# Optimization experiments

Hardware: AMD Instinct MI355X
Metric: run time of the kernel (lower is better)

Reference implementation:

```python
import jax, jax.numpy as jnp
import numpy as np

QB = 127.0  # act_bits=8 -> 2**(8-1)-1
EPS = 1e-5


def _ste(x, q):
    # straight-through estimator: forward = q, backward = identity
    return x + jax.lax.stop_gradient(q - x)


def bitlinear(x, W, b):
    """BitNet-b1.58 linear: ternary weights (per-tensor mean-abs scale),
    8-bit per-token absmax activations, dequantized matmul + bias."""
    w_scale = jnp.clip(jnp.mean(jnp.abs(W)), EPS, None)
    Wq = _ste(W, jnp.clip(jnp.round(W / w_scale), -1.0, 1.0) * w_scale)  # ternary * scale
    x_scale = jnp.clip(jnp.max(jnp.abs(x), axis=-1, keepdims=True), EPS, None)
    xq = _ste(x, jnp.clip(jnp.round(x * (QB / x_scale)), -QB - 1.0, QB) * (x_scale / QB))
    # x: [B, N, d_in], W: [d_out, d_in] -> [B, N, d_out]
    return jnp.einsum('bnd,hd->bnh', xq, Wq) + b


def setup_inputs() -> dict:
    key = jax.random.key(0)
    k0, k1, k2 = jax.random.split(key, 3)
    B, N, D = 8, 4096, 1024
    H = int(D * 4.0)
    x = jax.random.normal(k0, (B, N, D), dtype=jnp.float32)
    W1 = jax.random.normal(k1, (H, D), dtype=jnp.float32) * 0.02
    b1 = jnp.zeros((H,), dtype=jnp.float32)
    W2 = jax.random.normal(k2, (D, H), dtype=jnp.float32) * 0.02
    b2 = jnp.zeros((D,), dtype=jnp.float32)
    return {"x": x, "W1": W1, "b1": b1, "W2": W2, "b2": b2}


def reference(x, W1, b1, W2, b2):
    h = bitlinear(x, W1, b1)                 # [B, N, H]
    h = jax.nn.gelu(h, approximate=False)    # torch nn.GELU default = exact erf
    # dropout with p=0.0 is identity
    return bitlinear(h, W2, b2)              # [B, N, D]
```

## Files before the change

kernel.cpp:

```cpp
#include <hip/hip_runtime.h>
#include <hip/hip_bf16.h>
#include <math.h>


typedef int int32x4 __attribute__((ext_vector_type(4)));

typedef const void __attribute__((address_space(1))) gv_t;
typedef void __attribute__((address_space(3))) lv_t;

__device__ __forceinline__ void gload_lds16(const signed char* g,
                                            signed char* l) {
  __builtin_amdgcn_global_load_lds((gv_t*)g, (lv_t*)l, 16, 0, 0);
}

__device__ __forceinline__ float gelu_erf(float v) {
  return 0.5f * v * (1.0f + erff(v * 0.70710678118654752440f));
}

__device__ __forceinline__ void store_gt(float* p, float v) { *p = v; }
__device__ __forceinline__ void store_gt(__hip_bfloat16* p, float v) {
  unsigned u = __float_as_uint(v);
  u += 0x7fffu + ((u >> 16) & 1u);
  *(unsigned short*)p = (unsigned short)(u >> 16);
}

__device__ __forceinline__ void load4v(const float* p, float v[4]) {
  const float4 t = *(const float4*)p;
  v[0] = t.x; v[1] = t.y; v[2] = t.z; v[3] = t.w;
}
__device__ __forceinline__ void load4v(const __hip_bfloat16* p, float v[4]) {
  const ushort4 t = *(const ushort4*)p;
  v[0] = __uint_as_float((unsigned)t.x << 16);
  v[1] = __uint_as_float((unsigned)t.y << 16);
  v[2] = __uint_as_float((unsigned)t.z << 16);
  v[3] = __uint_as_float((unsigned)t.w << 16);
}

__global__ __launch_bounds__(256) void absmean_partial(
    const float* __restrict__ W, double* __restrict__ part) {
  const int tid = threadIdx.x;
  const long base = (long)blockIdx.x * 8192;
  double s = 0.0;
#pragma unroll
  for (int c = 0; c < 8; ++c) {
    const float4 v = *(const float4*)&W[base + c * 1024 + tid * 4];
    s += (double)fabsf(v.x) + (double)fabsf(v.y) +
         (double)fabsf(v.z) + (double)fabsf(v.w);
  }
  __shared__ double sm[256];
  sm[tid] = s; __syncthreads();
  for (int off = 128; off; off >>= 1) {
    if (tid < off) sm[tid] += sm[tid + off];
    __syncthreads();
  }
  if (tid == 0) part[blockIdx.x] = sm[0];
}

__global__ __launch_bounds__(256) void absmean_final(
    const double* __restrict__ part, double* __restrict__ out, double n) {
  const int tid = threadIdx.x;
  __shared__ double sm[256];
  sm[tid] = part[tid] + part[tid + 256];
  __syncthreads();
  for (int off = 128; off; off >>= 1) {
    if (tid < off) sm[tid] += sm[tid + off];
    __syncthreads();
  }
  if (tid == 0) out[0] = fmax(sm[0] / n, 1e-5);
}

__global__ __launch_bounds__(256) void quant_w(
    const float* __restrict__ W, const double* __restrict__ wsP,
    signed char* __restrict__ Wq) {
  const double ws = *wsP;
  const long i = ((long)blockIdx.x * 256 + threadIdx.x) * 4;
  const float4 v = *(const float4*)&W[i];
  const float vv[4] = {v.x, v.y, v.z, v.w};
  int pack = 0;
#pragma unroll
  for (int q = 0; q < 4; ++q) {
    double r = rint((double)vv[q] / ws);
    r = fmin(fmax(r, -1.0), 1.0);
    pack |= (((int)r) & 0xff) << (8 * q);
  }
  *(int*)&Wq[i] = pack;
}

template <int L, bool GELU, typename GT>
__global__ __launch_bounds__(256) void quant_rows(
    const GT* __restrict__ X, signed char* __restrict__ Xq,
    float* __restrict__ dsc) {
  constexpr int CH = L / 1024;
  const long row = blockIdx.x;
  const int tid = threadIdx.x;
  const GT* xr = X + row * (long)L;
  float v[CH][4];
  float m = 0.f;
#pragma unroll
  for (int c = 0; c < CH; ++c) {
    load4v(xr + c * 1024 + tid * 4, v[c]);
#pragma unroll
    for (int q = 0; q < 4; ++q) {
      if (GELU) v[c][q] = gelu_erf(v[c][q]);
      m = fmaxf(m, fabsf(v[c][q]));
    }
  }
#pragma unroll
  for (int off = 32; off; off >>= 1) m = fmaxf(m, __shfl_down(m, off, 64));
  __shared__ float wmx[4];
  if ((tid & 63) == 0) wmx[tid >> 6] = m;
  __syncthreads();
  float ms = fmaxf(fmaxf(wmx[0], wmx[1]), fmaxf(wmx[2], wmx[3]));
  ms = fmaxf(ms, 1e-5f);
  const double inv = 127.0 / (double)ms;
#pragma unroll
  for (int c = 0; c < CH; ++c) {
    int pack = 0;
#pragma unroll
    for (int q = 0; q < 4; ++q) {
      double r = rint((double)v[c][q] * inv);
      r = fmin(fmax(r, -128.0), 127.0);
      pack |= (((int)r) & 0xff) << (8 * q);
    }
    *(int*)&Xq[row * (long)L + c * 1024 + tid * 4] = pack;
  }
  if (tid == 0) dsc[row] = (float)((double)ms / 127.0);
}

template <typename GT>
__global__ __launch_bounds__(512, 2) void gemm_i8_256(
    const signed char* __restrict__ A, const signed char* __restrict__ Bm,
    const float* __restrict__ dA, const double* __restrict__ wsB,
    const float* __restrict__ bias, GT* __restrict__ C,
    int K, int Ncol, int nx) {
  __shared__ signed char LDS[131072];
  const int tid = threadIdx.x;
  const int lane = tid & 63;
  const int wave = tid >> 6;
  const int wm = wave >> 2;
  const int wn = wave & 3;

  const int cpx = gridDim.x >> 3;
  const int wg = ((int)blockIdx.x & 7) * cpx + ((int)blockIdx.x >> 3);
  const long rowBase = (long)(wg / nx) * 256;
  const long colBase = (long)(wg % nx) * 256;
  const int NT = K >> 6;

  const int d0 = tid << 4;
  const int r0 = d0 >> 6;
  const int c0 = (d0 & 63) ^ (((d0 >> 7) & 3) << 4);
  const signed char* gA0 = A + (rowBase + r0) * (long)K + c0;
  const signed char* gA1 = A + (rowBase + r0 + 128) * (long)K + c0;
  const signed char* gB0 = Bm + (colBase + r0) * (long)K + c0;
  const signed char* gB1 = Bm + (colBase + r0 + 128) * (long)K + c0;

  auto STAGE = [&](int tt) {
    const int bb = (tt & 3) << 14;
    const int k0 = tt << 6;
    gload_lds16(gA0 + k0, &LDS[bb + d0]);
    gload_lds16(gA1 + k0, &LDS[bb + d0 + 8192]);
    gload_lds16(gB0 + k0, &LDS[65536 + bb + d0]);
    gload_lds16(gB1 + k0, &LDS[65536 + bb + d0 + 8192]);
  };

  const int rl = lane & 15;
  const int kc = (lane >> 4) << 4;
  int aoff[8], boff[4];
#pragma unroll
  for (int mi = 0; mi < 8; ++mi) {
    const int a = (wm * 128 + mi * 16 + rl) * 64 + kc;
    aoff[mi] = a ^ (((a >> 7) & 3) << 4);
  }
#pragma unroll
  for (int nj = 0; nj < 4; ++nj) {
    const int a = (wn * 64 + nj * 16 + rl) * 64 + kc;
    boff[nj] = a ^ (((a >> 7) & 3) << 4);
  }

  int32x4 acc[8][4] = {};
  STAGE(0); STAGE(1); STAGE(2);

  for (int t = 0; t < NT; ++t) {
    if (t < NT - 2)       asm volatile("s_waitcnt vmcnt(8)" ::: "memory");
    else if (t == NT - 2) asm volatile("s_waitcnt vmcnt(4)" ::: "memory");
    else                  asm volatile("s_waitcnt vmcnt(0)" ::: "memory");
    __builtin_amdgcn_s_barrier();
    if (t + 3 < NT) STAGE(t + 3);

    const signed char* As = &LDS[(t & 3) << 14];
    const signed char* Bs = &LDS[65536 + ((t & 3) << 14)];
    int32x4 af[8], bf[4];
#pragma unroll
    for (int nj = 0; nj < 4; ++nj) bf[nj] = *(const int32x4*)&Bs[boff[nj]];
#pragma unroll
    for (int mi = 0; mi < 8; ++mi) af[mi] = *(const int32x4*)&As[aoff[mi]];
    __builtin_amdgcn_s_setprio(1);
#pragma unroll
    for (int mi = 0; mi < 8; ++mi)
#pragma unroll
      for (int nj = 0; nj < 4; ++nj)
        acc[mi][nj] = __builtin_amdgcn_mfma_i32_16x16x64_i8(
            af[mi], bf[nj], acc[mi][nj], 0, 0, 0);
    __builtin_amdgcn_s_setprio(0);
  }

  const double wsd = *wsB;
  const int rq = (lane >> 4) << 2;
  float bv[4];
#pragma unroll
  for (int nj = 0; nj < 4; ++nj)
    bv[nj] = bias[colBase + wn * 64 + nj * 16 + rl];
#pragma unroll
  for (int mi = 0; mi < 8; ++mi) {
#pragma unroll
    for (int r = 0; r < 4; ++r) {
      const long row = rowBase + wm * 128 + mi * 16 + rq + r;
      const float sc = (float)((double)dA[row] * wsd);
      GT* crow = C + row * (long)Ncol + colBase + wn * 64 + rl;
#pragma unroll
      for (int nj = 0; nj < 4; ++nj)
        store_gt(&crow[nj * 16], (float)acc[mi][nj][r] * sc + bv[nj]);
    }
  }
}

extern "C" void kernel_launch(void* const* d_in, const int* in_sizes, int n_in,
                              void* d_out, int out_size, void* d_ws,
                              size_t ws_size, hipStream_t stream) {
  const float* x  = (const float*)d_in[0];
  const float* W1 = (const float*)d_in[1];
  const float* b1 = (const float*)d_in[2];
  const float* W2 = (const float*)d_in[3];
  const float* b2 = (const float*)d_in[4];
  const int D = in_sizes[4];
  const int H = in_sizes[2];
  const long M = (long)in_sizes[0] / D;
  float* out = (float*)d_out;

  if (D != 1024 || H != 4096 || (M % 256) != 0) return;

  char* wsp = (char*)d_ws;
  size_t off = 0;
  auto alloc = [&](size_t bytes) {
    void* p = wsp + off;
    off = (off + bytes + 255) & ~(size_t)255;
    return p;
  };
  signed char* wq1 = (signed char*)alloc((size_t)H * D);
  signed char* wq2 = (signed char*)alloc((size_t)D * H);
  signed char* xq  = (signed char*)alloc((size_t)M * D);
  signed char* gq  = (signed char*)alloc((size_t)M * H);
  float* dx = (float*)alloc((size_t)M * 4);
  float* dg = (float*)alloc((size_t)M * 4);
  double* part = (double*)alloc(512 * 8);
  double* ws1 = (double*)alloc(8);
  double* ws2 = (double*)alloc(8);
  const size_t g_f32_bytes = (size_t)M * H * 4;
  const bool g32 = (off + g_f32_bytes) <= ws_size;
  const size_t g_bytes = g32 ? g_f32_bytes : (size_t)M * H * 2;
  if (off + g_bytes > ws_size) return;
  void* g = alloc(g_bytes);

  const long nW = (long)H * D;
  absmean_partial<<<nW / 8192, 256, 0, stream>>>(W1, part);
  absmean_final<<<1, 256, 0, stream>>>(part, ws1, (double)nW);
  absmean_partial<<<nW / 8192, 256, 0, stream>>>(W2, part);
  absmean_final<<<1, 256, 0, stream>>>(part, ws2, (double)nW);
  quant_w<<<nW / 1024, 256, 0, stream>>>(W1, ws1, wq1);
  quant_w<<<nW / 1024, 256, 0, stream>>>(W2, ws2, wq2);
  quant_rows<1024, false, float><<<M, 256, 0, stream>>>(x, xq, dx);

  const int g1 = (H / 256) * (int)(M / 256);
  const int g2 = (D / 256) * (int)(M / 256);
  if (g32) {
    gemm_i8_256<float><<<g1, 512, 0, stream>>>(
        xq, wq1, dx, ws1, b1, (float*)g, D, H, H / 256);
    quant_rows<4096, true, float><<<M, 256, 0, stream>>>(
        (const float*)g, gq, dg);
  } else {
    gemm_i8_256<__hip_bfloat16><<<g1, 512, 0, stream>>>(
        xq, wq1, dx, ws1, b1, (__hip_bfloat16*)g, D, H, H / 256);
    quant_rows<4096, true, __hip_bfloat16><<<M, 256, 0, stream>>>(
        (const __hip_bfloat16*)g, gq, dg);
  }
  gemm_i8_256<float><<<g2, 512, 0, stream>>>(
      gq, wq2, dg, ws2, b2, out, H, D, D / 256);
}
```

Baseline: 477.4 us.

## Restructure int8 GEMM into 8-phase K=128 pipeline and always use bf16 intermediate

The int8 GEMM now loads 128-wide K tiles with double buffering, split into separate A and B stages. Each tile is processed in four sub-phases that interleave LDS fragment loads, barriers and MFMA groups, with the next tile's global-to-LDS copies issued partway through. The goal is better overlap of memory traffic and MFMA work and fewer loop iterations. Separately, the hidden activation is now always stored in bf16 instead of fp32 when space allows, which halves the intermediate write/read traffic at some extra rounding risk before requantization.

Result: faster. 462.3 us (-3.2%).

```diff
diff --git a/kernel.cpp b/kernel.cpp
--- a/kernel.cpp
+++ b/kernel.cpp
@@ -128,7 +128,7 @@
 }
 
 template <typename GT>
-__global__ __launch_bounds__(512, 2) void gemm_i8_256(
+__global__ __launch_bounds__(512, 2) void gemm_i8_8ph(
     const signed char* __restrict__ A, const signed char* __restrict__ Bm,
     const float* __restrict__ dA, const double* __restrict__ wsB,
     const float* __restrict__ bias, GT* __restrict__ C,
@@ -144,64 +144,101 @@
   const int wg = ((int)blockIdx.x & 7) * cpx + ((int)blockIdx.x >> 3);
   const long rowBase = (long)(wg / nx) * 256;
   const long colBase = (long)(wg % nx) * 256;
-  const int NT = K >> 6;
-
-  const int d0 = tid << 4;
-  const int r0 = d0 >> 6;
-  const int c0 = (d0 & 63) ^ (((d0 >> 7) & 3) << 4);
-  const signed char* gA0 = A + (rowBase + r0) * (long)K + c0;
-  const signed char* gA1 = A + (rowBase + r0 + 128) * (long)K + c0;
-  const signed char* gB0 = Bm + (colBase + r0) * (long)K + c0;
-  const signed char* gB1 = Bm + (colBase + r0 + 128) * (long)K + c0;
-
-  auto STAGE = [&](int tt) {
-    const int bb = (tt & 3) << 14;
-    const int k0 = tt << 6;
-    gload_lds16(gA0 + k0, &LDS[bb + d0]);
-    gload_lds16(gA1 + k0, &LDS[bb + d0 + 8192]);
-    gload_lds16(gB0 + k0, &LDS[65536 + bb + d0]);
-    gload_lds16(gB1 + k0, &LDS[65536 + bb + d0 + 8192]);
+  const int NT = K >> 7;
+
+  const int dd = wave * 1024 + lane * 16;
+  const int srow = dd >> 7;
+  const int scol = (dd & 127) ^ ((srow & 7) << 4);
+  const long k64 = 64L * K;
+  const signed char* sA0 = A + (rowBase + srow) * (long)K + scol;
+  const signed char* sB0 = Bm + (colBase + srow) * (long)K + scol;
+
+  auto STAGE_A = [&](int t) {
+    const signed char* p = sA0 + ((long)t << 7);
+    signed char* l = &LDS[((t & 1) << 15) + dd];
+#pragma unroll
+    for (int i = 0; i < 4; ++i) gload_lds16(p + i * k64, l + i * 8192);
   };
+  auto STAGE_B = [&](int t) {
+    const signed char* p = sB0 + ((long)t << 7);
+    signed char* l = &LDS[65536 + ((t & 1) << 15) + dd];
+#pragma unroll
+    for (int i = 0; i < 4; ++i) gload_lds16(p + i * k64, l + i * 8192);
+  };
 
   const int rl = lane & 15;
-  const int kc = (lane >> 4) << 4;
-  int aoff[8], boff[4];
-#pragma unroll
-  for (int mi = 0; mi < 8; ++mi) {
-    const int a = (wm * 128 + mi * 16 + rl) * 64 + kc;
-    aoff[mi] = a ^ (((a >> 7) & 3) << 4);
-  }
-#pragma unroll
-  for (int nj = 0; nj < 4; ++nj) {
-    const int a = (wn * 64 + nj * 16 + rl) * 64 + kc;
-    boff[nj] = a ^ (((a >> 7) & 3) << 4);
-  }
+  const int col0 = (((lane >> 4) << 4)) ^ ((rl & 7) << 4);
+  const int aRow = wm * 16384 + rl * 128;
+  const int bRow = wn * 8192 + rl * 128;
 
   int32x4 acc[8][4] = {};
-  STAGE(0); STAGE(1); STAGE(2);
+
+  STAGE_B(0); STAGE_A(0); STAGE_B(1);
+  asm volatile("s_waitcnt vmcnt(4)" ::: "memory");
+  __builtin_amdgcn_s_barrier();
 
   for (int t = 0; t < NT; ++t) {
-    if (t < NT - 2)       asm volatile("s_waitcnt vmcnt(8)" ::: "memory");
-    else if (t == NT - 2) asm volatile("s_waitcnt vmcnt(4)" ::: "memory");
-    else                  asm volatile("s_waitcnt vmcnt(0)" ::: "memory");
-    __builtin_amdgcn_s_barrier();
-    if (t + 3 < NT) STAGE(t + 3);
-
-    const signed char* As = &LDS[(t & 3) << 14];
-    const signed char* Bs = &LDS[65536 + ((t & 3) << 14)];
-    int32x4 af[8], bf[4];
-#pragma unroll
-    for (int nj = 0; nj < 4; ++nj) bf[nj] = *(const int32x4*)&Bs[boff[nj]];
-#pragma unroll
-    for (int mi = 0; mi < 8; ++mi) af[mi] = *(const int32x4*)&As[aoff[mi]];
+    const signed char* At = &LDS[(t & 1) << 15];
+    const signed char* Bt = &LDS[65536 + ((t & 1) << 15)];
+    int32x4 af[4], bf[4];
+
+    auto LDA = [&](int mih, int kc6) {
+#pragma unroll
+      for (int i = 0; i < 4; ++i)
+        af[i] = *(const int32x4*)(At + aRow + (mih * 4 + i) * 2048 +
+                                  (col0 ^ kc6));
+    };
+    auto LDB = [&](int kc6) {
+#pragma unroll
+      for (int nj = 0; nj < 4; ++nj)
+        bf[nj] = *(const int32x4*)(Bt + bRow + nj * 2048 + (col0 ^ kc6));
+    };
+    auto MFMA16 = [&](int mih) {
+#pragma unroll
+      for (int i = 0; i < 4; ++i)
+#pragma unroll
+        for (int nj = 0; nj < 4; ++nj)
+          acc[mih * 4 + i][nj] = __builtin_amdgcn_mfma_i32_16x16x64_i8(
+              af[i], bf[nj], acc[mih * 4 + i][nj], 0, 0, 0);
+    };
+
+    LDB(0);
+    LDA(0, 0);
+    if (t + 1 < NT) STAGE_A(t + 1);
+    __builtin_amdgcn_s_barrier();
     __builtin_amdgcn_s_setprio(1);
-#pragma unroll
-    for (int mi = 0; mi < 8; ++mi)
-#pragma unroll
-      for (int nj = 0; nj < 4; ++nj)
-        acc[mi][nj] = __builtin_amdgcn_mfma_i32_16x16x64_i8(
-            af[mi], bf[nj], acc[mi][nj], 0, 0, 0);
+    MFMA16(0);
     __builtin_amdgcn_s_setprio(0);
+    asm volatile("s_waitcnt lgkmcnt(0)" ::: "memory");
+    __builtin_amdgcn_s_barrier();
+
+    LDA(1, 0);
+    __builtin_amdgcn_s_barrier();
+    __builtin_amdgcn_s_setprio(1);
+    MFMA16(1);
+    __builtin_amdgcn_s_setprio(0);
+    asm volatile("s_waitcnt lgkmcnt(0)" ::: "memory");
+    __builtin_amdgcn_s_barrier();
+
+    LDB(64);
+    LDA(0, 64);
+    __builtin_amdgcn_s_barrier();
+    __builtin_amdgcn_s_setprio(1);
+    MFMA16(0);
+    __builtin_amdgcn_s_setprio(0);
+    asm volatile("s_waitcnt lgkmcnt(0)" ::: "memory");
+    __builtin_amdgcn_s_barrier();
+
+    LDA(1, 64);
+    if (t + 2 < NT) STAGE_B(t + 2);
+    if (t < NT - 2) asm volatile("s_waitcnt vmcnt(4)" ::: "memory");
+    else            asm volatile("s_waitcnt vmcnt(0)" ::: "memory");
+    __builtin_amdgcn_s_barrier();
+    __builtin_amdgcn_s_setprio(1);
+    MFMA16(1);
+    __builtin_amdgcn_s_setprio(0);
+    asm volatile("s_waitcnt lgkmcnt(0)" ::: "memory");
+    __builtin_amdgcn_s_barrier();
   }
 
   const double wsd = *wsB;
@@ -255,11 +292,8 @@
   double* part = (double*)alloc(512 * 8);
   double* ws1 = (double*)alloc(8);
   double* ws2 = (double*)alloc(8);
-  const size_t g_f32_bytes = (size_t)M * H * 4;
-  const bool g32 = (off + g_f32_bytes) <= ws_size;
-  const size_t g_bytes = g32 ? g_f32_bytes : (size_t)M * H * 2;
-  if (off + g_bytes > ws_size) return;
-  void* g = alloc(g_bytes);
+  __hip_bfloat16* h = (__hip_bfloat16*)alloc((size_t)M * H * 2);
+  if (off > ws_size) return;
 
   const long nW = (long)H * D;
   absmean_partial<<<nW / 8192, 256, 0, stream>>>(W1, part);
@@ -272,17 +306,9 @@
 
   const int g1 = (H / 256) * (int)(M / 256);
   const int g2 = (D / 256) * (int)(M / 256);
-  if (g32) {
-    gemm_i8_256<float><<<g1, 512, 0, stream>>>(
-        xq, wq1, dx, ws1, b1, (float*)g, D, H, H / 256);
-    quant_rows<4096, true, float><<<M, 256, 0, stream>>>(
-        (const float*)g, gq, dg);
-  } else {
-    gemm_i8_256<__hip_bfloat16><<<g1, 512, 0, stream>>>(
-        xq, wq1, dx, ws1, b1, (__hip_bfloat16*)g, D, H, H / 256);
-    quant_rows<4096, true, __hip_bfloat16><<<M, 256, 0, stream>>>(
-        (const __hip_bfloat16*)g, gq, dg);
-  }
-  gemm_i8_256<float><<<g2, 512, 0, stream>>>(
+  gemm_i8_8ph<__hip_bfloat16><<<g1, 512, 0, stream>>>(
+      xq, wq1, dx, ws1, b1, h, D, H, H / 256);
+  quant_rows<4096, true, __hip_bfloat16><<<M, 256, 0, stream>>>(h, gq, dg);
+  gemm_i8_8ph<float><<<g2, 512, 0, stream>>>(
       gq, wq2, dg, ws2, b2, out, H, D, D / 256);
 }
```
